# Kernel tuning notes

Measured on AMD Instinct MI355X. Metric: run time of the kernel, lower is better.

The kernel has to match this reference:

```python
import jax, jax.numpy as jnp
import numpy as np

N = 50000      # nodes
E = 600000     # edges
F_IN = 128     # num_features
H = 128        # conv_dim
C = 10         # num_classes


def setup_inputs() -> dict:
    key = jax.random.key(0)
    ks = jax.random.split(key, 16)
    s = 0.05
    return {
        "x": jax.random.normal(ks[0], (N, F_IN), jnp.float32),
        "edge_index": jax.random.randint(ks[1], (2, E), 0, N, dtype=jnp.int32),
        "W1": jax.random.normal(ks[2], (F_IN, H), jnp.float32) * s,
        "b1": jnp.zeros((H,), jnp.float32),
        "W2": jax.random.normal(ks[3], (H, H), jnp.float32) * s,
        "b2": jnp.zeros((H,), jnp.float32),
        "W3": jax.random.normal(ks[4], (H, H), jnp.float32) * s,
        "b3": jnp.zeros((H,), jnp.float32),
        "fw1": jax.random.normal(ks[5], (3 * H, 128), jnp.float32) * s,
        "fb1": jnp.zeros((128,), jnp.float32),
        "fw2": jax.random.normal(ks[6], (128, 64), jnp.float32) * s,
        "fb2": jnp.zeros((64,), jnp.float32),
        "fw3": jax.random.normal(ks[7], (64, C), jnp.float32) * s,
        "fb3": jnp.zeros((C,), jnp.float32),
    }


def reference(x, edge_index, W1, b1, W2, b2, W3, b3, fw1, fb1, fw2, fb2, fw3, fb3):
    n = x.shape[0]
    # GCN normalization with self-loops (improved=False): A_hat = D^-1/2 (A+I) D^-1/2
    loop = jnp.arange(n, dtype=edge_index.dtype)
    src = jnp.concatenate([edge_index[0], loop])   # [E+N]
    tgt = jnp.concatenate([edge_index[1], loop])   # [E+N]
    deg = jax.ops.segment_sum(jnp.ones_like(src, dtype=x.dtype), tgt, num_segments=n)
    dis = jnp.where(deg > 0, jax.lax.rsqrt(jnp.maximum(deg, 1e-12)), 0.0)
    norm = dis[src] * dis[tgt]                     # [E+N]

    def gcn(h, W, b):
        hw = h @ W                                 # [N,H] linear transform first
        msg = norm[:, None] * hw[src]              # gather + edge scale
        return jax.ops.segment_sum(msg, tgt, num_segments=n) + b  # scatter-add

    x1 = jax.nn.relu(gcn(x, W1, b1))
    x2 = jax.nn.relu(gcn(x1, W2, b2))
    x3 = jax.nn.relu(gcn(x2, W3, b3))
    h = jnp.sum(jnp.concatenate([x1, x2, x3], axis=1), axis=0)  # [3H] sum pool
    h = jax.nn.relu(h @ fw1 + fb1)
    h = jax.nn.relu(h @ fw2 + fb2)
    return h @ fw3 + fb3
```

## Files before the change

kernel.cpp:

```cpp
#include <hip/hip_runtime.h>

#define FDIM 128

typedef __attribute__((ext_vector_type(8))) short bf16x8;
typedef __attribute__((ext_vector_type(4))) float f32x4;
typedef __attribute__((ext_vector_type(2))) float f32x2;


__device__ __forceinline__ unsigned int cvt_bf16(float f) {
    unsigned int u = __float_as_uint(f);
    return (u + 0x7fffu + ((u >> 16) & 1u)) >> 16;
}



__global__ void hist_kernel(const int* __restrict__ tgt, int* __restrict__ count, int ne) {
    int e = blockIdx.x * blockDim.x + threadIdx.x;
    if (e < ne) atomicAdd(&count[tgt[e]], 1);
}

__global__ __launch_bounds__(256) void scan1_kernel(const int* __restrict__ count,
                                                    float* __restrict__ dis,
                                                    int* __restrict__ tpre,
                                                    int* __restrict__ bsum, int n) {
    __shared__ int sm[256];
    int tid = threadIdx.x, blk = blockIdx.x;
    int base = blk * 2048 + tid * 8;
    int s = 0;
    #pragma unroll
    for (int q = 0; q < 8; q++) {
        int i = base + q;
        if (i < n) {
            int c = count[i];
            s += c;
            dis[i] = rsqrtf((float)(c + 1));
        }
    }
    sm[tid] = s;
    __syncthreads();
    for (int off = 1; off < 256; off <<= 1) {
        int v = sm[tid];
        int u = (tid >= off) ? sm[tid - off] : 0;
        __syncthreads();
        sm[tid] = v + u;
        __syncthreads();
    }
    tpre[blk * 256 + tid] = (tid == 0) ? 0 : sm[tid - 1];
    if (tid == 255) bsum[blk] = sm[255];
}

__global__ __launch_bounds__(1024) void scan2_kernel(const int* __restrict__ bsum,
                                                     int* __restrict__ bpre,
                                                     int* __restrict__ rowptr,
                                                     float* __restrict__ pool,
                                                     int n, int nb) {
    __shared__ int sm[1024];
    int tid = threadIdx.x;
    if (tid < 384) pool[tid] = 0.f;
    sm[tid] = (tid < nb) ? bsum[tid] : 0;
    __syncthreads();
    for (int off = 1; off < 1024; off <<= 1) {
        int v = sm[tid];
        int u = (tid >= off) ? sm[tid - off] : 0;
        __syncthreads();
        sm[tid] = v + u;
        __syncthreads();
    }
    if (tid < nb) bpre[tid] = (tid == 0) ? 0 : sm[tid - 1];
    if (tid == nb - 1) rowptr[n] = sm[tid];
}

__global__ __launch_bounds__(256) void scan3_kernel(const int* __restrict__ count,
                                                    const int* __restrict__ tpre,
                                                    const int* __restrict__ bpre,
                                                    int* __restrict__ rowptr,
                                                    int* __restrict__ cursor, int n) {
    int tid = threadIdx.x, blk = blockIdx.x;
    int run = bpre[blk] + tpre[blk * 256 + tid];
    int base = blk * 2048 + tid * 8;
    #pragma unroll
    for (int q = 0; q < 8; q++) {
        int i = base + q;
        if (i < n) {
            rowptr[i] = run;
            cursor[i] = run;
            run += count[i];
        }
    }
}

__global__ void fill_kernel(const int* __restrict__ src, const int* __restrict__ tgt,
                            int* __restrict__ cursor, int* __restrict__ csrs, int ne) {
    int e = blockIdx.x * blockDim.x + threadIdx.x;
    if (e < ne) {
        int t = tgt[e];
        int s = src[e];
        int slot = atomicAdd(&cursor[t], 1);
        csrs[slot] = s;
    }
}


__global__ void prep_kernel(const float* __restrict__ W1, const float* __restrict__ W2,
                            const float* __restrict__ W3,
                            unsigned* __restrict__ B1, unsigned* __restrict__ B2,
                            unsigned* __restrict__ B3,
                            unsigned short* __restrict__ g8,
                            int* __restrict__ count, int n) {
    int i = blockIdx.x * blockDim.x + threadIdx.x;
    if (i < 3 * 8192) {
        int w = i >> 13;
        int jj = i & 8191;
        const float* W = (w == 0) ? W1 : (w == 1) ? W2 : W3;
        unsigned* B    = (w == 0) ? B1 : (w == 1) ? B2 : B3;
        int nn = jj >> 6, u = jj & 63;
        float lo = W[(size_t)u * 128 + nn];
        float hi = W[(size_t)(u + 64) * 128 + nn];
        B[jj] = cvt_bf16(lo) | (cvt_bf16(hi) << 16);
    } else if (i < 3 * 8192 + 64) {
        g8[(size_t)n * 64 + (i - 3 * 8192)] = 0;
    } else {
        int k = i - (3 * 8192 + 64);
        if (k < n) count[k] = 0;
    }
}


__global__ __launch_bounds__(256) void gemm_kernel(const unsigned* __restrict__ A16,
                                                   const float* __restrict__ A32,
                                                   const unsigned* __restrict__ Bt16,
                                                   const float* __restrict__ dis,
                                                   unsigned short* __restrict__ g8, int n) {
    int tid  = threadIdx.x;
    int wave = tid >> 6, lane = tid & 63;
    int quad = lane >> 4, r16 = lane & 15;
    int m0 = (blockIdx.x * 4 + wave) * 16;
    if (m0 >= n) return;

    f32x4 acc[8] = {};

    #pragma unroll
    for (int ks = 0; ks < 4; ks++) {
        int m = m0 + r16;
        if (m >= n) m = n - 1;
        int u0 = ks * 16 + quad * 4;
        bf16x8 af;
        if (A32) {
            float4 lo = *(const float4*)(A32 + (size_t)m * 128 + u0);
            float4 hi = *(const float4*)(A32 + (size_t)m * 128 + u0 + 64);
            uint4 p;
            p.x = cvt_bf16(lo.x) | (cvt_bf16(hi.x) << 16);
            p.y = cvt_bf16(lo.y) | (cvt_bf16(hi.y) << 16);
            p.z = cvt_bf16(lo.z) | (cvt_bf16(hi.z) << 16);
            p.w = cvt_bf16(lo.w) | (cvt_bf16(hi.w) << 16);
            af = *(bf16x8*)&p;
        } else {
            uint4 av = *(const uint4*)(A16 + (size_t)m * 64 + u0);
            af = *(bf16x8*)&av;
        }
        #pragma unroll
        for (int t = 0; t < 8; t++) {
            int ncol = t * 16 + r16;
            uint4 bv = *(const uint4*)(Bt16 + (size_t)ncol * 64 + u0);
            bf16x8 bf = *(bf16x8*)&bv;
            acc[t] = __builtin_amdgcn_mfma_f32_16x16x32_bf16(af, bf, acc[t], 0, 0, 0);
        }
    }

    #pragma unroll
    for (int r = 0; r < 4; r++) {
        int row = m0 + quad * 4 + r;
        if (row < n) {
            float dr = dis[row];
            #pragma unroll
            for (int t = 0; t < 4; t++) {
                int p = __builtin_amdgcn_cvt_pk_fp8_f32(dr * acc[t][r], dr * acc[t + 4][r], 0, false);
                g8[(size_t)row * 64 + t * 16 + r16] = (unsigned short)(p & 0xffff);
            }
        }
    }
}


#define AGG_ACC(v)                                                     \
    { f32x2 p;                                                         \
      p = __builtin_amdgcn_cvt_pk_f32_fp8((int)v.x, 0); f0[0]+=p.x; f1[0]+=p.y; \
      p = __builtin_amdgcn_cvt_pk_f32_fp8((int)v.x, 1); f0[1]+=p.x; f1[1]+=p.y; \
      p = __builtin_amdgcn_cvt_pk_f32_fp8((int)v.y, 0); f0[2]+=p.x; f1[2]+=p.y; \
      p = __builtin_amdgcn_cvt_pk_f32_fp8((int)v.y, 1); f0[3]+=p.x; f1[3]+=p.y; \
      p = __builtin_amdgcn_cvt_pk_f32_fp8((int)v.z, 0); f0[4]+=p.x; f1[4]+=p.y; \
      p = __builtin_amdgcn_cvt_pk_f32_fp8((int)v.z, 1); f0[5]+=p.x; f1[5]+=p.y; \
      p = __builtin_amdgcn_cvt_pk_f32_fp8((int)v.w, 0); f0[6]+=p.x; f1[6]+=p.y; \
      p = __builtin_amdgcn_cvt_pk_f32_fp8((int)v.w, 1); f0[7]+=p.x; f1[7]+=p.y; }

#define ISSUE1(buf, ereg, EBASE, mlim)                                 \
    { int e = (EBASE) + j;                                             \
      int s = __shfl(ereg, e);                                         \
      if (e >= (mlim)) s = n;                                          \
      buf = *(const uint4*)(g8 + (size_t)(unsigned)s * 64u + c * 8); }

#define ROUND4(ereg, Q0, mlim)                                         \
    { uint4 u0, u1, u2, u3;                                            \
      ISSUE1(u0, ereg, (Q0) + 0, mlim)                                 \
      if ((mlim) > (Q0) + 8)  ISSUE1(u1, ereg, (Q0) + 8,  mlim)        \
      if ((mlim) > (Q0) + 16) ISSUE1(u2, ereg, (Q0) + 16, mlim)        \
      if ((mlim) > (Q0) + 24) ISSUE1(u3, ereg, (Q0) + 24, mlim)        \
      AGG_ACC(u0)                                                      \
      if ((mlim) > (Q0) + 8)  AGG_ACC(u1)                              \
      if ((mlim) > (Q0) + 16) AGG_ACC(u2)                              \
      if ((mlim) > (Q0) + 24) AGG_ACC(u3) }

__global__ __launch_bounds__(512) void agg_kernel(const unsigned short* __restrict__ g8,
                                                  const float* __restrict__ dis,
                                                  const int* __restrict__ rowptr,
                                                  const int* __restrict__ csrs,
                                                  const float* __restrict__ bias,
                                                  unsigned* __restrict__ out16,
                                                  float* __restrict__ pool,
                                                  int n, int nbase, int nend) {
    __shared__ float lpool[128];
    int tid = threadIdx.x;
    if (tid < 128) lpool[tid] = 0.f;
    __syncthreads();

    int wave = tid >> 6, lane = tid & 63;
    int j = lane >> 3;
    int c = lane & 7;
    int node0 = nbase + (blockIdx.x * 8 + wave) * 4;

    float b0[8], b1[8];
    *(float4*)&b0[0] = *(const float4*)(bias + c * 8);
    *(float4*)&b0[4] = *(const float4*)(bias + c * 8 + 4);
    *(float4*)&b1[0] = *(const float4*)(bias + 64 + c * 8);
    *(float4*)&b1[4] = *(const float4*)(bias + 64 + c * 8 + 4);

    int rpv = 0; float dv = 0.f;
    if (lane <= 4) rpv = rowptr[min(node0 + lane, nend)];
    if (lane < 4)  dv  = dis[min(node0 + lane, n - 1)];

    int er[4];
    #pragma unroll
    for (int i = 0; i < 4; i++) {
        int beg = __shfl(rpv, i);
        er[i] = csrs[beg + lane];
    }

    uint4 c0, c1, c2, c3, sB;
    {
        int deg = __shfl(rpv, 1) - __shfl(rpv, 0);
        int mlim = min(deg, 64);
        int ereg = er[0];
        ISSUE1(c0, ereg, 0, mlim)
        if (deg > 8)  ISSUE1(c1, ereg, 8,  mlim)
        if (deg > 16) ISSUE1(c2, ereg, 16, mlim)
        if (deg > 24) ISSUE1(c3, ereg, 24, mlim)
        int s = (node0 < nend && j == 0) ? node0 : n;
        sB = *(const uint4*)(g8 + (size_t)(unsigned)s * 64u + c * 8);
    }

    float pp0[8] = {}, pp1[8] = {};

    #pragma unroll
    for (int i = 0; i < 4; i++) {
        int node = node0 + i;
        bool ok = node < nend;
        int beg = __shfl(rpv, i);
        int end = __shfl(rpv, i + 1);
        int deg = end - beg;
        float di = __shfl(dv, i);

        float f0[8] = {}, f1[8] = {};
        AGG_ACC(c0)
        if (deg > 8)  AGG_ACC(c1)
        if (deg > 16) AGG_ACC(c2)
        if (deg > 24) AGG_ACC(c3)
        if (deg > 32) {
            int mlim = min(deg, 64);
            ROUND4(er[i], 32, mlim)
            for (int b2 = 64; b2 < deg; b2 += 64) {
                int ereg2 = csrs[beg + b2 + lane];
                int ml2 = min(deg - b2, 64);
                ROUND4(ereg2, 0, ml2)
                if (ml2 > 32) ROUND4(ereg2, 32, ml2)
            }
        }

        uint4 n0v, n1v, n2v, n3v, nS;
        if (i < 3) {
            int nd = __shfl(rpv, i + 2) - end;
            int nml = min(nd, 64);
            int ner = er[i + 1];
            ISSUE1(n0v, ner, 0, nml)
            if (nd > 8)  ISSUE1(n1v, ner, 8,  nml)
            if (nd > 16) ISSUE1(n2v, ner, 16, nml)
            if (nd > 24) ISSUE1(n3v, ner, 24, nml)
            int s = (node + 1 < nend && j == 0) ? (node + 1) : n;
            nS = *(const uint4*)(g8 + (size_t)(unsigned)s * 64u + c * 8);
        }

        #pragma unroll
        for (int k = 0; k < 8; k++) {
            f0[k] += __shfl_xor(f0[k], 8);  f1[k] += __shfl_xor(f1[k], 8);
            f0[k] += __shfl_xor(f0[k], 16); f1[k] += __shfl_xor(f1[k], 16);
            f0[k] += __shfl_xor(f0[k], 32); f1[k] += __shfl_xor(f1[k], 32);
        }
        if (j == 0) AGG_ACC(sB)

        if (ok) {
            float r0[8], r1[8];
            #pragma unroll
            for (int k = 0; k < 8; k++) {
                r0[k] = fmaxf(di * f0[k] + b0[k], 0.f);
                r1[k] = fmaxf(di * f1[k] + b1[k], 0.f);
                pp0[k] += r0[k];
                pp1[k] += r1[k];
            }
            if (out16 && j == 0) {
                uint4 wa, wb;
                wa.x = cvt_bf16(r0[0]) | (cvt_bf16(r1[0]) << 16);
                wa.y = cvt_bf16(r0[1]) | (cvt_bf16(r1[1]) << 16);
                wa.z = cvt_bf16(r0[2]) | (cvt_bf16(r1[2]) << 16);
                wa.w = cvt_bf16(r0[3]) | (cvt_bf16(r1[3]) << 16);
                wb.x = cvt_bf16(r0[4]) | (cvt_bf16(r1[4]) << 16);
                wb.y = cvt_bf16(r0[5]) | (cvt_bf16(r1[5]) << 16);
                wb.z = cvt_bf16(r0[6]) | (cvt_bf16(r1[6]) << 16);
                wb.w = cvt_bf16(r0[7]) | (cvt_bf16(r1[7]) << 16);
                *(uint4*)(out16 + (size_t)node * 64 + c * 8)     = wa;
                *(uint4*)(out16 + (size_t)node * 64 + c * 8 + 4) = wb;
            }
        }

        c0 = n0v; c1 = n1v; c2 = n2v; c3 = n3v; sB = nS;
    }

    if (j == 0) {
        #pragma unroll
        for (int k = 0; k < 8; k++) {
            atomicAdd(&lpool[c * 8 + k],      pp0[k]);
            atomicAdd(&lpool[64 + c * 8 + k], pp1[k]);
        }
    }
    __syncthreads();
    if (tid < 128) atomicAdd(&pool[tid], lpool[tid]);
}


__global__ __launch_bounds__(128) void mlp_kernel(const float* __restrict__ pool,
                                                  const float* __restrict__ fw1, const float* __restrict__ fb1,
                                                  const float* __restrict__ fw2, const float* __restrict__ fb2,
                                                  const float* __restrict__ fw3, const float* __restrict__ fb3,
                                                  float* __restrict__ out) {
    __shared__ float h0[384];
    __shared__ float h1[128];
    __shared__ float h2[64];
    int tid = threadIdx.x;
    for (int i = tid; i < 384; i += 128) h0[i] = pool[i];
    __syncthreads();
    {
        float s = fb1[tid];
        for (int k = 0; k < 384; k++) s += h0[k] * fw1[k * 128 + tid];
        h1[tid] = fmaxf(s, 0.f);
    }
    __syncthreads();
    if (tid < 64) {
        float s = fb2[tid];
        for (int k = 0; k < 128; k++) s += h1[k] * fw2[k * 64 + tid];
        h2[tid] = fmaxf(s, 0.f);
    }
    __syncthreads();
    if (tid < 10) {
        float s = fb3[tid];
        for (int k = 0; k < 64; k++) s += h2[k] * fw3[k * 10 + tid];
        out[tid] = s;
    }
}


extern "C" void kernel_launch(void* const* d_in, const int* in_sizes, int n_in,
                              void* d_out, int out_size, void* d_ws, size_t ws_size,
                              hipStream_t stream) {
    const float* x   = (const float*)d_in[0];
    const int*   ei  = (const int*)d_in[1];
    const float* W1  = (const float*)d_in[2];
    const float* b1  = (const float*)d_in[3];
    const float* W2  = (const float*)d_in[4];
    const float* b2  = (const float*)d_in[5];
    const float* W3  = (const float*)d_in[6];
    const float* b3  = (const float*)d_in[7];
    const float* fw1 = (const float*)d_in[8];
    const float* fb1 = (const float*)d_in[9];
    const float* fw2 = (const float*)d_in[10];
    const float* fb2 = (const float*)d_in[11];
    const float* fw3 = (const float*)d_in[12];
    const float* fb3 = (const float*)d_in[13];
    float* out = (float*)d_out;

    const int n  = in_sizes[0] / FDIM;
    const int ne = in_sizes[1] / 2;
    const int* src = ei;
    const int* tgt = ei + ne;

    char* ws = (char*)d_ws;
    size_t packBytes = (size_t)n * 64 * sizeof(unsigned);
    unsigned* A2   = (unsigned*)ws;  ws += packBytes;
    unsigned* A3   = (unsigned*)ws;  ws += packBytes;
    unsigned short* g8 = (unsigned short*)ws; ws += (((size_t)(n + 1) * 64 * 2 + 127) / 128) * 128;
    unsigned* B1t  = (unsigned*)ws;  ws += 128 * 64 * 4;
    unsigned* B2t  = (unsigned*)ws;  ws += 128 * 64 * 4;
    unsigned* B3t  = (unsigned*)ws;  ws += 128 * 64 * 4;
    float* dis  = (float*)ws;        ws += (size_t)n * 4;
    int* count  = (int*)ws;          ws += (size_t)n * 4;
    int* rowptr = (int*)ws;          ws += ((size_t)(n + 4) * 4 / 16) * 16;
    int* cursor = (int*)ws;          ws += (size_t)n * 4;
    int* csrs   = (int*)ws;          ws += (size_t)(ne + 64) * 4;
    float* pool = (float*)ws;        ws += 384 * 4;
    int nb = (n + 2047) / 2048;
    int* tpre = (int*)ws;            ws += (size_t)nb * 256 * 4;
    int* bsum = (int*)ws;            ws += ((size_t)(nb + 3) / 4) * 16;
    int* bpre = (int*)ws;            ws += ((size_t)(nb + 3) / 4) * 16;

    int prepTotal = 3 * 8192 + 64 + n;
    prep_kernel<<<(prepTotal + 255) / 256, 256, 0, stream>>>(W1, W2, W3, B1t, B2t, B3t, g8, count, n);

    hist_kernel<<<(ne + 255) / 256, 256, 0, stream>>>(tgt, count, ne);
    scan1_kernel<<<nb, 256, 0, stream>>>(count, dis, tpre, bsum, n);
    scan2_kernel<<<1, 1024, 0, stream>>>(bsum, bpre, rowptr, pool, n, nb);
    scan3_kernel<<<nb, 256, 0, stream>>>(count, tpre, bpre, rowptr, cursor, n);
    fill_kernel<<<(ne + 255) / 256, 256, 0, stream>>>(src, tgt, cursor, csrs, ne);

    int gemmGrid = (n + 63) / 64;
    int half = ((n / 2) + 31) & ~31;
    int ag1 = (half + 31) / 32;
    int ag2 = ((n - half) + 31) / 32;

    gemm_kernel<<<gemmGrid, 256, 0, stream>>>((const unsigned*)nullptr, x, B1t, dis, g8, n);
    agg_kernel<<<ag1, 512, 0, stream>>>(g8, dis, rowptr, csrs, b1, A2, pool + 0, n, 0, half);
    agg_kernel<<<ag2, 512, 0, stream>>>(g8, dis, rowptr, csrs, b1, A2, pool + 0, n, half, n);

    gemm_kernel<<<gemmGrid, 256, 0, stream>>>(A2, (const float*)nullptr, B2t, dis, g8, n);
    agg_kernel<<<ag1, 512, 0, stream>>>(g8, dis, rowptr, csrs, b2, A3, pool + 128, n, 0, half);
    agg_kernel<<<ag2, 512, 0, stream>>>(g8, dis, rowptr, csrs, b2, A3, pool + 128, n, half, n);

    gemm_kernel<<<gemmGrid, 256, 0, stream>>>(A3, (const float*)nullptr, B3t, dis, g8, n);
    agg_kernel<<<ag1, 512, 0, stream>>>(g8, dis, rowptr, csrs, b3, (unsigned*)nullptr, pool + 256, n, 0, half);
    agg_kernel<<<ag2, 512, 0, stream>>>(g8, dis, rowptr, csrs, b3, (unsigned*)nullptr, pool + 256, n, half, n);

    mlp_kernel<<<1, 128, 0, stream>>>(pool, fw1, fb1, fw2, fb2, fw3, fb3, out);
}
```

Before: 512.2 us.

## Merge preprocessing and GCN stages into fewer kernel launches

Cuts the launch count by merging kernels. Weight packing is fused with the degree histogram, and the three-pass scan becomes one kernel where the last-arriving block computes block prefixes and the others spin-wait on a flag. Edge fill now runs alongside the first GEMM in one grid, the split aggregation launches are unified, and the MLP head runs in the last aggregation block via an atomic counter. GEMM blocks grow to 512 threads covering 128 rows, and zeroing uses hipMemsetAsync. The inter-block spin-wait relies on all scan blocks being co-resident, and the fill blocks now compete with GEMM blocks for the GPU.

```diff
diff --git a/kernel.cpp b/kernel.cpp
--- a/kernel.cpp
+++ b/kernel.cpp
@@ -6,7 +6,6 @@
 typedef __attribute__((ext_vector_type(4))) float f32x4;
 typedef __attribute__((ext_vector_type(2))) float f32x2;
 
-
 __device__ __forceinline__ unsigned int cvt_bf16(float f) {
     unsigned int u = __float_as_uint(f);
     return (u + 0x7fffu + ((u >> 16) & 1u)) >> 16;
@@ -14,26 +13,53 @@
 
 
 
-__global__ void hist_kernel(const int* __restrict__ tgt, int* __restrict__ count, int ne) {
-    int e = blockIdx.x * blockDim.x + threadIdx.x;
-    if (e < ne) atomicAdd(&count[tgt[e]], 1);
-}
-
-__global__ __launch_bounds__(256) void scan1_kernel(const int* __restrict__ count,
-                                                    float* __restrict__ dis,
-                                                    int* __restrict__ tpre,
-                                                    int* __restrict__ bsum, int n) {
+__global__ void prephist_kernel(const float* __restrict__ W1, const float* __restrict__ W2,
+                                const float* __restrict__ W3,
+                                unsigned* __restrict__ B1, unsigned* __restrict__ B2,
+                                unsigned* __restrict__ B3,
+                                unsigned short* __restrict__ g8,
+                                const int* __restrict__ tgt, int* __restrict__ count,
+                                int n, int ne) {
+    int i = blockIdx.x * blockDim.x + threadIdx.x;
+    if (i < 24576) {
+        int w = i >> 13, jj = i & 8191;
+        const float* W = (w == 0) ? W1 : (w == 1) ? W2 : W3;
+        unsigned* B    = (w == 0) ? B1 : (w == 1) ? B2 : B3;
+        int nn = jj >> 6, u = jj & 63;
+        float lo = W[(size_t)u * 128 + nn];
+        float hi = W[(size_t)(u + 64) * 128 + nn];
+        B[jj] = cvt_bf16(lo) | (cvt_bf16(hi) << 16);
+    } else if (i < 24640) {
+        g8[(size_t)n * 64 + (i - 24576)] = 0;
+    } else {
+        int e = i - 24640;
+        if (e < ne) atomicAdd(&count[tgt[e]], 1);
+    }
+}
+
+
+__global__ __launch_bounds__(256) void scan_kernel(const int* __restrict__ count,
+                                                   float* __restrict__ dis,
+                                                   int* __restrict__ rowptr,
+                                                   int* __restrict__ cursor,
+                                                   int* __restrict__ bsum,
+                                                   int* __restrict__ bpre,
+                                                   int* __restrict__ ctrs,
+                                                   int n, int nb) {
     __shared__ int sm[256];
+    __shared__ int sbase;
     int tid = threadIdx.x, blk = blockIdx.x;
     int base = blk * 2048 + tid * 8;
+    int c[8];
     int s = 0;
     #pragma unroll
     for (int q = 0; q < 8; q++) {
         int i = base + q;
+        c[q] = 0;
         if (i < n) {
-            int c = count[i];
-            s += c;
-            dis[i] = rsqrtf((float)(c + 1));
+            c[q] = count[i];
+            s += c[q];
+            dis[i] = rsqrtf((float)(c[q] + 1));
         }
     }
     sm[tid] = s;
@@ -45,100 +71,54 @@
         sm[tid] = v + u;
         __syncthreads();
     }
-    tpre[blk * 256 + tid] = (tid == 0) ? 0 : sm[tid - 1];
-    if (tid == 255) bsum[blk] = sm[255];
-}
-
-__global__ __launch_bounds__(1024) void scan2_kernel(const int* __restrict__ bsum,
-                                                     int* __restrict__ bpre,
-                                                     int* __restrict__ rowptr,
-                                                     float* __restrict__ pool,
-                                                     int n, int nb) {
-    __shared__ int sm[1024];
-    int tid = threadIdx.x;
-    if (tid < 384) pool[tid] = 0.f;
-    sm[tid] = (tid < nb) ? bsum[tid] : 0;
-    __syncthreads();
-    for (int off = 1; off < 1024; off <<= 1) {
-        int v = sm[tid];
-        int u = (tid >= off) ? sm[tid - off] : 0;
-        __syncthreads();
-        sm[tid] = v + u;
-        __syncthreads();
-    }
-    if (tid < nb) bpre[tid] = (tid == 0) ? 0 : sm[tid - 1];
-    if (tid == nb - 1) rowptr[n] = sm[tid];
-}
-
-__global__ __launch_bounds__(256) void scan3_kernel(const int* __restrict__ count,
-                                                    const int* __restrict__ tpre,
-                                                    const int* __restrict__ bpre,
-                                                    int* __restrict__ rowptr,
-                                                    int* __restrict__ cursor, int n) {
-    int tid = threadIdx.x, blk = blockIdx.x;
-    int run = bpre[blk] + tpre[blk * 256 + tid];
-    int base = blk * 2048 + tid * 8;
+    int tpre = sm[tid] - s;
+    int btot = sm[255];
+    __syncthreads();
+
+    if (tid == 0) {
+        __hip_atomic_store(&bsum[blk], btot, __ATOMIC_RELAXED, __HIP_MEMORY_SCOPE_AGENT);
+        __threadfence();
+        int old = atomicAdd(&ctrs[0], 1);
+        if (old == nb - 1) {
+            int run = 0;
+            for (int b = 0; b < nb; b++) {
+                int v = __hip_atomic_load(&bsum[b], __ATOMIC_RELAXED, __HIP_MEMORY_SCOPE_AGENT);
+                __hip_atomic_store(&bpre[b], run, __ATOMIC_RELAXED, __HIP_MEMORY_SCOPE_AGENT);
+                run += v;
+            }
+            rowptr[n] = run;
+            __threadfence();
+            __hip_atomic_store(&ctrs[1], 1, __ATOMIC_RELEASE, __HIP_MEMORY_SCOPE_AGENT);
+        }
+        while (__hip_atomic_load(&ctrs[1], __ATOMIC_ACQUIRE, __HIP_MEMORY_SCOPE_AGENT) == 0) {}
+        sbase = __hip_atomic_load(&bpre[blk], __ATOMIC_RELAXED, __HIP_MEMORY_SCOPE_AGENT);
+    }
+    __syncthreads();
+    int run = sbase + tpre;
     #pragma unroll
     for (int q = 0; q < 8; q++) {
         int i = base + q;
         if (i < n) {
             rowptr[i] = run;
             cursor[i] = run;
-            run += count[i];
-        }
-    }
-}
-
-__global__ void fill_kernel(const int* __restrict__ src, const int* __restrict__ tgt,
-                            int* __restrict__ cursor, int* __restrict__ csrs, int ne) {
-    int e = blockIdx.x * blockDim.x + threadIdx.x;
-    if (e < ne) {
-        int t = tgt[e];
-        int s = src[e];
-        int slot = atomicAdd(&cursor[t], 1);
-        csrs[slot] = s;
-    }
-}
-
-
-__global__ void prep_kernel(const float* __restrict__ W1, const float* __restrict__ W2,
-                            const float* __restrict__ W3,
-                            unsigned* __restrict__ B1, unsigned* __restrict__ B2,
-                            unsigned* __restrict__ B3,
-                            unsigned short* __restrict__ g8,
-                            int* __restrict__ count, int n) {
-    int i = blockIdx.x * blockDim.x + threadIdx.x;
-    if (i < 3 * 8192) {
-        int w = i >> 13;
-        int jj = i & 8191;
-        const float* W = (w == 0) ? W1 : (w == 1) ? W2 : W3;
-        unsigned* B    = (w == 0) ? B1 : (w == 1) ? B2 : B3;
-        int nn = jj >> 6, u = jj & 63;
-        float lo = W[(size_t)u * 128 + nn];
-        float hi = W[(size_t)(u + 64) * 128 + nn];
-        B[jj] = cvt_bf16(lo) | (cvt_bf16(hi) << 16);
-    } else if (i < 3 * 8192 + 64) {
-        g8[(size_t)n * 64 + (i - 3 * 8192)] = 0;
-    } else {
-        int k = i - (3 * 8192 + 64);
-        if (k < n) count[k] = 0;
-    }
-}
-
-
-__global__ __launch_bounds__(256) void gemm_kernel(const unsigned* __restrict__ A16,
-                                                   const float* __restrict__ A32,
-                                                   const unsigned* __restrict__ Bt16,
-                                                   const float* __restrict__ dis,
-                                                   unsigned short* __restrict__ g8, int n) {
-    int tid  = threadIdx.x;
+            run += c[q];
+        }
+    }
+}
+
+
+__device__ __forceinline__ void gemm_body(const unsigned* __restrict__ A16,
+                                          const float* __restrict__ A32,
+                                          const unsigned* __restrict__ Bt16,
+                                          const float* __restrict__ dis,
+                                          unsigned short* __restrict__ g8,
+                                          int n, int T) {
+    int tid = threadIdx.x;
     int wave = tid >> 6, lane = tid & 63;
     int quad = lane >> 4, r16 = lane & 15;
-    int m0 = (blockIdx.x * 4 + wave) * 16;
+    int m0 = T * 128 + wave * 16;
     if (m0 >= n) return;
-
     f32x4 acc[8] = {};
-
     #pragma unroll
     for (int ks = 0; ks < 4; ks++) {
         int m = m0 + r16;
@@ -166,7 +146,6 @@
             acc[t] = __builtin_amdgcn_mfma_f32_16x16x32_bf16(af, bf, acc[t], 0, 0, 0);
         }
     }
-
     #pragma unroll
     for (int r = 0; r < 4; r++) {
         int row = m0 + quad * 4 + r;
@@ -179,6 +158,37 @@
             }
         }
     }
+}
+
+
+__global__ __launch_bounds__(512) void fillgemm_kernel(const int* __restrict__ src,
+                                                       const int* __restrict__ tgt,
+                                                       int* __restrict__ cursor,
+                                                       int* __restrict__ csrs,
+                                                       const float* __restrict__ x,
+                                                       const unsigned* __restrict__ B1t,
+                                                       const float* __restrict__ dis,
+                                                       unsigned short* __restrict__ g8,
+                                                       int n, int ne, int nG, int nF) {
+    if ((int)blockIdx.x < nG) {
+        gemm_body(nullptr, x, B1t, dis, g8, n, blockIdx.x);
+    } else {
+        int b = blockIdx.x - nG;
+        for (int e = b * 512 + threadIdx.x; e < ne; e += nF * 512) {
+            int t = tgt[e];
+            int s = src[e];
+            int slot = atomicAdd(&cursor[t], 1);
+            csrs[slot] = s;
+        }
+    }
+}
+
+
+__global__ __launch_bounds__(512) void gemm_kernel(const unsigned* __restrict__ A16,
+                                                   const unsigned* __restrict__ Bt16,
+                                                   const float* __restrict__ dis,
+                                                   unsigned short* __restrict__ g8, int n) {
+    gemm_body(A16, nullptr, Bt16, dis, g8, n, blockIdx.x);
 }
 
 
@@ -210,15 +220,14 @@
       if ((mlim) > (Q0) + 16) AGG_ACC(u2)                              \
       if ((mlim) > (Q0) + 24) AGG_ACC(u3) }
 
-__global__ __launch_bounds__(512) void agg_kernel(const unsigned short* __restrict__ g8,
-                                                  const float* __restrict__ dis,
-                                                  const int* __restrict__ rowptr,
-                                                  const int* __restrict__ csrs,
-                                                  const float* __restrict__ bias,
-                                                  unsigned* __restrict__ out16,
-                                                  float* __restrict__ pool,
-                                                  int n, int nbase, int nend) {
-    __shared__ float lpool[128];
+__device__ __forceinline__ void agg_body(const unsigned short* __restrict__ g8,
+                                         const float* __restrict__ dis,
+                                         const int* __restrict__ rowptr,
+                                         const int* __restrict__ csrs,
+                                         const float* __restrict__ bias,
+                                         unsigned* __restrict__ out16,
+                                         float* __restrict__ poolseg,
+                                         float* lpool, int n) {
     int tid = threadIdx.x;
     if (tid < 128) lpool[tid] = 0.f;
     __syncthreads();
@@ -226,7 +235,7 @@
     int wave = tid >> 6, lane = tid & 63;
     int j = lane >> 3;
     int c = lane & 7;
-    int node0 = nbase + (blockIdx.x * 8 + wave) * 4;
+    int node0 = (blockIdx.x * 8 + wave) * 4;
 
     float b0[8], b1[8];
     *(float4*)&b0[0] = *(const float4*)(bias + c * 8);
@@ -235,7 +244,7 @@
     *(float4*)&b1[4] = *(const float4*)(bias + 64 + c * 8 + 4);
 
     int rpv = 0; float dv = 0.f;
-    if (lane <= 4) rpv = rowptr[min(node0 + lane, nend)];
+    if (lane <= 4) rpv = rowptr[min(node0 + lane, n)];
     if (lane < 4)  dv  = dis[min(node0 + lane, n - 1)];
 
     int er[4];
@@ -254,7 +263,7 @@
         if (deg > 8)  ISSUE1(c1, ereg, 8,  mlim)
         if (deg > 16) ISSUE1(c2, ereg, 16, mlim)
         if (deg > 24) ISSUE1(c3, ereg, 24, mlim)
-        int s = (node0 < nend && j == 0) ? node0 : n;
+        int s = (node0 < n && j == 0) ? node0 : n;
         sB = *(const uint4*)(g8 + (size_t)(unsigned)s * 64u + c * 8);
     }
 
@@ -263,7 +272,7 @@
     #pragma unroll
     for (int i = 0; i < 4; i++) {
         int node = node0 + i;
-        bool ok = node < nend;
+        bool ok = node < n;
         int beg = __shfl(rpv, i);
         int end = __shfl(rpv, i + 1);
         int deg = end - beg;
@@ -294,7 +303,7 @@
             if (nd > 8)  ISSUE1(n1v, ner, 8,  nml)
             if (nd > 16) ISSUE1(n2v, ner, 16, nml)
             if (nd > 24) ISSUE1(n3v, ner, 24, nml)
-            int s = (node + 1 < nend && j == 0) ? (node + 1) : n;
+            int s = (node + 1 < n && j == 0) ? (node + 1) : n;
             nS = *(const uint4*)(g8 + (size_t)(unsigned)s * 64u + c * 8);
         }
 
@@ -329,7 +338,6 @@
                 *(uint4*)(out16 + (size_t)node * 64 + c * 8 + 4) = wb;
             }
         }
-
         c0 = n0v; c1 = n1v; c2 = n2v; c3 = n3v; sB = nS;
     }
 
@@ -341,22 +349,52 @@
         }
     }
     __syncthreads();
-    if (tid < 128) atomicAdd(&pool[tid], lpool[tid]);
-}
-
-
-__global__ __launch_bounds__(128) void mlp_kernel(const float* __restrict__ pool,
-                                                  const float* __restrict__ fw1, const float* __restrict__ fb1,
-                                                  const float* __restrict__ fw2, const float* __restrict__ fb2,
-                                                  const float* __restrict__ fw3, const float* __restrict__ fb3,
-                                                  float* __restrict__ out) {
+    if (tid < 128) atomicAdd(&poolseg[tid], lpool[tid]);
+}
+
+__global__ __launch_bounds__(512) void agg_kernel(const unsigned short* __restrict__ g8,
+                                                  const float* __restrict__ dis,
+                                                  const int* __restrict__ rowptr,
+                                                  const int* __restrict__ csrs,
+                                                  const float* __restrict__ bias,
+                                                  unsigned* __restrict__ out16,
+                                                  float* __restrict__ poolseg, int n) {
+    __shared__ float lpool[128];
+    agg_body(g8, dis, rowptr, csrs, bias, out16, poolseg, lpool, n);
+}
+
+__global__ __launch_bounds__(512) void aggmlp_kernel(const unsigned short* __restrict__ g8,
+                                                     const float* __restrict__ dis,
+                                                     const int* __restrict__ rowptr,
+                                                     const int* __restrict__ csrs,
+                                                     const float* __restrict__ bias,
+                                                     float* __restrict__ pool,
+                                                     int* __restrict__ ctrs,
+                                                     const float* __restrict__ fw1, const float* __restrict__ fb1,
+                                                     const float* __restrict__ fw2, const float* __restrict__ fb2,
+                                                     const float* __restrict__ fw3, const float* __restrict__ fb3,
+                                                     float* __restrict__ out, int n) {
+    __shared__ float lpool[128];
     __shared__ float h0[384];
     __shared__ float h1[128];
     __shared__ float h2[64];
+    __shared__ int slast;
+
+    agg_body(g8, dis, rowptr, csrs, bias, (unsigned*)nullptr, pool + 256, lpool, n);
+
     int tid = threadIdx.x;
-    for (int i = tid; i < 384; i += 128) h0[i] = pool[i];
-    __syncthreads();
-    {
+    if (tid == 0) {
+        __threadfence();
+        int old = atomicAdd(&ctrs[2], 1);
+        slast = (old == (int)gridDim.x - 1) ? 1 : 0;
+    }
+    __syncthreads();
+    if (!slast) return;
+
+    for (int i = tid; i < 384; i += 512)
+        h0[i] = __hip_atomic_load(&pool[i], __ATOMIC_RELAXED, __HIP_MEMORY_SCOPE_AGENT);
+    __syncthreads();
+    if (tid < 128) {
         float s = fb1[tid];
         for (int k = 0; k < 384; k++) s += h0[k] * fw1[k * 128 + tid];
         h1[tid] = fmaxf(s, 0.f);
@@ -410,40 +448,34 @@
     unsigned* B3t  = (unsigned*)ws;  ws += 128 * 64 * 4;
     float* dis  = (float*)ws;        ws += (size_t)n * 4;
     int* count  = (int*)ws;          ws += (size_t)n * 4;
+    int* ctrs   = (int*)ws;          ws += 8 * 4;
+    float* pool = (float*)ws;        ws += 384 * 4;
     int* rowptr = (int*)ws;          ws += ((size_t)(n + 4) * 4 / 16) * 16;
     int* cursor = (int*)ws;          ws += (size_t)n * 4;
     int* csrs   = (int*)ws;          ws += (size_t)(ne + 64) * 4;
-    float* pool = (float*)ws;        ws += 384 * 4;
+    int* bsum   = (int*)ws;          ws += 32 * 4;
+    int* bpre   = (int*)ws;          ws += 32 * 4;
+
+    hipMemsetAsync(count, 0, (size_t)(n + 8 + 384) * 4, stream);
+
+    int phTotal = 24640 + ne;
+    prephist_kernel<<<(phTotal + 255) / 256, 256, 0, stream>>>(W1, W2, W3, B1t, B2t, B3t,
+                                                               g8, tgt, count, n, ne);
+
     int nb = (n + 2047) / 2048;
-    int* tpre = (int*)ws;            ws += (size_t)nb * 256 * 4;
-    int* bsum = (int*)ws;            ws += ((size_t)(nb + 3) / 4) * 16;
-    int* bpre = (int*)ws;            ws += ((size_t)(nb + 3) / 4) * 16;
-
-    int prepTotal = 3 * 8192 + 64 + n;
-    prep_kernel<<<(prepTotal + 255) / 256, 256, 0, stream>>>(W1, W2, W3, B1t, B2t, B3t, g8, count, n);
-
-    hist_kernel<<<(ne + 255) / 256, 256, 0, stream>>>(tgt, count, ne);
-    scan1_kernel<<<nb, 256, 0, stream>>>(count, dis, tpre, bsum, n);
-    scan2_kernel<<<1, 1024, 0, stream>>>(bsum, bpre, rowptr, pool, n, nb);
-    scan3_kernel<<<nb, 256, 0, stream>>>(count, tpre, bpre, rowptr, cursor, n);
-    fill_kernel<<<(ne + 255) / 256, 256, 0, stream>>>(src, tgt, cursor, csrs, ne);
-
-    int gemmGrid = (n + 63) / 64;
-    int half = ((n / 2) + 31) & ~31;
-    int ag1 = (half + 31) / 32;
-    int ag2 = ((n - half) + 31) / 32;
-
-    gemm_kernel<<<gemmGrid, 256, 0, stream>>>((const unsigned*)nullptr, x, B1t, dis, g8, n);
-    agg_kernel<<<ag1, 512, 0, stream>>>(g8, dis, rowptr, csrs, b1, A2, pool + 0, n, 0, half);
-    agg_kernel<<<ag2, 512, 0, stream>>>(g8, dis, rowptr, csrs, b1, A2, pool + 0, n, half, n);
-
-    gemm_kernel<<<gemmGrid, 256, 0, stream>>>(A2, (const float*)nullptr, B2t, dis, g8, n);
-    agg_kernel<<<ag1, 512, 0, stream>>>(g8, dis, rowptr, csrs, b2, A3, pool + 128, n, 0, half);
-    agg_kernel<<<ag2, 512, 0, stream>>>(g8, dis, rowptr, csrs, b2, A3, pool + 128, n, half, n);
-
-    gemm_kernel<<<gemmGrid, 256, 0, stream>>>(A3, (const float*)nullptr, B3t, dis, g8, n);
-    agg_kernel<<<ag1, 512, 0, stream>>>(g8, dis, rowptr, csrs, b3, (unsigned*)nullptr, pool + 256, n, 0, half);
-    agg_kernel<<<ag2, 512, 0, stream>>>(g8, dis, rowptr, csrs, b3, (unsigned*)nullptr, pool + 256, n, half, n);
-
-    mlp_kernel<<<1, 128, 0, stream>>>(pool, fw1, fb1, fw2, fb2, fw3, fb3, out);
-}
+    scan_kernel<<<nb, 256, 0, stream>>>(count, dis, rowptr, cursor, bsum, bpre, ctrs, n, nb);
+
+    int nG = (n + 127) / 128;
+    int nF = 128;
+    fillgemm_kernel<<<nG + nF, 512, 0, stream>>>(src, tgt, cursor, csrs, x, B1t, dis, g8,
+                                                 n, ne, nG, nF);
+
+    int aggGrid = (n + 31) / 32;
+
+    agg_kernel<<<aggGrid, 512, 0, stream>>>(g8, dis, rowptr, csrs, b1, A2, pool + 0, n);
+    gemm_kernel<<<nG, 512, 0, stream>>>(A2, B2t, dis, g8, n);
+    agg_kernel<<<aggGrid, 512, 0, stream>>>(g8, dis, rowptr, csrs, b2, A3, pool + 128, n);
+    gemm_kernel<<<nG, 512, 0, stream>>>(A3, B3t, dis, g8, n);
+    aggmlp_kernel<<<aggGrid, 512, 0, stream>>>(g8, dis, rowptr, csrs, b3, pool, ctrs,
+                                               fw1, fb1, fw2, fb2, fw3, fb3, out, n);
+}
```

After: 460.8 us. -10.0%, faster.
